# Kernel optimization log

Measured on AMD Instinct MI355X. Metric: run time of the kernel, lower is better.

## Reference

```python
import jax, jax.numpy as jnp
import numpy as np

B, L, H, NH, DH, V, NL = 256, 100, 384, 12, 32, 30000, 6
FF = 4 * H


def _gelu(x):
    c = np.sqrt(2.0 / np.pi).astype(np.float32)
    return x * (0.5 * (1.0 + jnp.tanh(c * (x + 0.044715 * x ** 3))))


def _norm(X, g, b):
    mu = jnp.mean(X, axis=2, keepdims=True)
    var = jnp.var(X, axis=2, ddof=1, keepdims=True)  # torch.var is unbiased
    return g * ((X - mu) / jnp.sqrt(var + 1e-8)) + b


def setup_inputs():
    key = jax.random.key(0)
    ks = jax.random.split(key, 24)
    s = 0.02
    return {
        'x': jax.random.randint(ks[0], (B, L), 0, V, dtype=jnp.int32),
        'seg': jax.random.randint(ks[1], (B, L), 0, 3, dtype=jnp.int32),
        'tok_emb': jax.random.uniform(ks[2], (V, H), jnp.float32, -s, s),
        'seg_emb': jax.random.uniform(ks[3], (3, H), jnp.float32, -s, s),
        'pos_emb': jax.random.normal(ks[4], (L, H), jnp.float32) * 0.05,
        'Wq': jax.random.normal(ks[5], (NL, H, H), jnp.float32) * np.sqrt(2.0 / H).astype(np.float32),
        'bq': jnp.zeros((NL, H), jnp.float32),
        'Wk': jax.random.normal(ks[6], (NL, H, H), jnp.float32) * np.sqrt(2.0 / H).astype(np.float32),
        'bk': jnp.zeros((NL, H), jnp.float32),
        'Wv': jax.random.normal(ks[7], (NL, H, H), jnp.float32) * np.sqrt(2.0 / H).astype(np.float32),
        'bv': jnp.zeros((NL, H), jnp.float32),
        'Wo': jax.random.normal(ks[8], (NL, H, H), jnp.float32) * np.sqrt(2.0 / (2 * H)).astype(np.float32),
        'bo': jnp.zeros((NL, H), jnp.float32),
        'g1': jnp.ones((NL,), jnp.float32),
        'be1': jnp.zeros((NL,), jnp.float32),
        'W1': jax.random.normal(ks[9], (NL, H, FF), jnp.float32) * np.sqrt(2.0 / (H + FF)).astype(np.float32),
        'b1': jnp.zeros((NL, FF), jnp.float32),
        'W2': jax.random.normal(ks[10], (NL, FF, H), jnp.float32) * np.sqrt(2.0 / (H + FF)).astype(np.float32),
        'b2': jnp.zeros((NL, H), jnp.float32),
        'g2': jnp.ones((NL,), jnp.float32),
        'be2': jnp.zeros((NL,), jnp.float32),
        'dropout': 0,
    }


def _encoder_layer(h, pad_mask, nonpad, Wq, bq, Wk, bk, Wv, bv, Wo, bo, g1, be1, W1, b1, W2, b2, g2, be2):
    # --- multi-head self-attention (interleaved head split, as in source) ---
    q = (h @ Wq + bq).reshape(B, L, DH, NH).transpose(3, 0, 1, 2)  # (NH,B,L,DH)
    k = (h @ Wk + bk).reshape(B, L, DH, NH).transpose(3, 0, 3 - 1, 1)  # placeholder
    k = (h @ Wk + bk).reshape(B, L, DH, NH).transpose(3, 0, 2, 1)      # (NH,B,DH,L)
    v = (h @ Wv + bv).reshape(B, L, DH, NH).transpose(3, 0, 1, 2)      # (NH,B,L,DH)
    scale = 1.0 / np.sqrt(H).astype(np.float32)  # d_k = de.shape[-1] = hidden_dim!
    e = jnp.einsum('hbld,hbdm->hblm', q, k) * scale                    # (NH,B,L,L)
    e = jnp.where(pad_mask[None], -1e10, e)
    alpha = jax.nn.softmax(e, axis=-1)
    heads = jnp.einsum('hblm,hbmd->hbld', alpha, v)                    # (NH,B,L,DH)
    a = heads.transpose(1, 2, 0, 3).reshape(B, L, H)  # cat over heads on feature dim
    attn = _norm(a @ Wo + bo + h, g1, be1)
    attn = attn * nonpad
    # --- FFN ---
    f = _gelu(attn @ W1 + b1)
    f = f @ W2 + b2
    out = _norm(f + attn, g2, be2)
    return out * nonpad


def reference(x, seg, tok_emb, seg_emb, pos_emb, Wq, bq, Wk, bk, Wv, bv, Wo, bo,
              g1, be1, W1, b1, W2, b2, g2, be2, dropout):
    pad_mask = (x == 0)[:, None, :] * jnp.ones((1, L, 1), bool)  # (B,L,L)
    nonpad = (x != 0).astype(jnp.float32)[:, :, None]            # (B,L,1), bcast over H
    h = tok_emb[x] + seg_emb[seg] + pos_emb[None, :L]
    h = h * nonpad
    acc = h  # cumulative-sum skip connections: input_i = x_i + ... + x_1
    out = h
    for i in range(NL):
        out = _encoder_layer(acc, pad_mask, nonpad,
                             Wq[i], bq[i], Wk[i], bk[i], Wv[i], bv[i], Wo[i], bo[i],
                             g1[i], be1[i], W1[i], b1[i], W2[i], b2[i], g2[i], be2[i])
        acc = acc + out
    return out
```

## Files before the change

kernel.cpp:

```cpp
#include <hip/hip_runtime.h>
#include <hip/hip_bf16.h>
#include <math.h>

#define B_  256
#define L_  100
#define H_  384
#define NH_ 12
#define DH_ 32
#define NL_ 6
#define FF_ 1536
#define M_  (B_*L_)
#define QKVN 1152

#define LW     3538944
#define OFF_Q  0
#define OFF_K  294912
#define OFF_V  589824
#define OFF_WO 884736
#define OFF_W1 1179648
#define OFF_W2 2359296

typedef __attribute__((ext_vector_type(8))) short short8;
typedef __attribute__((ext_vector_type(4))) float f32x4;

#define GLOBAL_AS __attribute__((address_space(1)))
#define LDS_AS    __attribute__((address_space(3)))

__device__ __forceinline__ void gload_lds16(const void* g, void* l) {
    __builtin_amdgcn_global_load_lds((const GLOBAL_AS void*)g, (LDS_AS void*)l, 16, 0, 0);
}

__device__ __forceinline__ void split2(float v, __hip_bfloat16& hi, __hip_bfloat16& lo) {
    hi = __float2bfloat16(v);
    lo = __float2bfloat16(v - __bfloat162float(hi));
}

__device__ __forceinline__ unsigned short f2b(float v) {
    __hip_bfloat16 h = __float2bfloat16(v);
    return *(unsigned short*)&h;
}

#define VMW(N) asm volatile("s_waitcnt vmcnt(" #N ")" ::: "memory")

__global__ void embed_kernel(const int* __restrict__ x, const int* __restrict__ seg,
                             const float* __restrict__ tok, const float* __restrict__ sege,
                             const float* __restrict__ pos,
                             __hip_bfloat16* __restrict__ acc2) {
    int idx = blockIdx.x * blockDim.x + threadIdx.x;
    if (idx >= M_ * H_) return;
    int m = idx / H_;
    int f = idx - m * H_;
    int t = x[m];
    int s = seg[m];
    int l = m % L_;
    float v = tok[t * H_ + f] + sege[s * H_ + f] + pos[l * H_ + f];
    v = (t != 0) ? v : 0.0f;
    __hip_bfloat16 h, lo;
    split2(v, h, lo);
    acc2[(size_t)m * (2 * H_) + f]      = h;
    acc2[(size_t)m * (2 * H_) + H_ + f] = lo;
}

__global__ void transpose_all_kernel(const float* __restrict__ Wq, const float* __restrict__ Wk,
        const float* __restrict__ Wv, const float* __restrict__ Wo,
        const float* __restrict__ W1, const float* __restrict__ W2,
        __hip_bfloat16* __restrict__ wT) {
    __shared__ float tile[32][33];
    int l = blockIdx.x / 1728;
    int bid = blockIdx.x % 1728;
    const float* src;
    __hip_bfloat16* dst;
    int K, N, nx, tix, perm = 0;
    if (bid < 432) {
        int m = bid / 144; tix = bid % 144;
        src = (m == 0) ? Wq : (m == 1 ? Wk : Wv);
        src += (size_t)l * H_ * H_;
        dst = wT + (size_t)l * LW + (m == 0 ? OFF_Q : (m == 1 ? OFF_K : OFF_V));
        K = 384; N = 384; nx = 12; perm = 1;
    } else if (bid < 576) {
        tix = bid - 432; src = Wo + (size_t)l * H_ * H_;
        dst = wT + (size_t)l * LW + OFF_WO; K = 384; N = 384; nx = 12;
    } else if (bid < 1152) {
        tix = bid - 576; src = W1 + (size_t)l * H_ * FF_;
        dst = wT + (size_t)l * LW + OFF_W1; K = 384; N = 1536; nx = 48;
    } else {
        tix = bid - 1152; src = W2 + (size_t)l * FF_ * H_;
        dst = wT + (size_t)l * LW + OFF_W2; K = 1536; N = 384; nx = 12;
    }
    int n0 = (tix % nx) * 32, k0 = (tix / nx) * 32;
    int tx = threadIdx.x, ty = threadIdx.y;
    #pragma unroll
    for (int i = ty; i < 32; i += 8)
        tile[i][tx] = src[(size_t)(k0 + i) * N + (n0 + tx)];
    __syncthreads();
    #pragma unroll
    for (int i = ty; i < 32; i += 8) {
        float v = tile[tx][i];
        __hip_bfloat16 h, lo;
        split2(v, h, lo);
        int j = n0 + i;
        int jo = perm ? ((j % 12) * 32 + j / 12) : j;
        dst[(size_t)jo * (2 * K) + (k0 + tx)]     = h;
        dst[(size_t)jo * (2 * K) + K + (k0 + tx)] = lo;
    }
}

__global__ void bias_concat_kernel(const float* __restrict__ bq, const float* __restrict__ bk,
                                   const float* __restrict__ bv, float* __restrict__ out) {
    int i = blockIdx.x * 256 + threadIdx.x;
    if (i >= NL_ * QKVN) return;
    int l = i / QKVN, jp = i - l * QKVN;
    int t = jp / 384, r = jp % 384;
    int h = r >> 5, d = r & 31;
    int j = d * 12 + h;
    float v = (t == 0) ? bq[l * 384 + j] : (t == 1 ? bk[l * 384 + j] : bv[l * 384 + j]);
    out[i] = v;
}

template <int TAG, int BIG, int OMODE, int MODEK, int ACT>
__global__ __launch_bounds__(BIG ? 512 : 256) void gemm_bf16_kernel(
        const __hip_bfloat16* __restrict__ A2,
        const __hip_bfloat16* __restrict__ Wt2,
        const float* __restrict__ bias,
        void* __restrict__ outp,
        int N, int K, int nbx) {
    constexpr int BM = BIG ? 256 : 128;
    __shared__ __hip_bfloat16 As[3][BM * 32];
    __shared__ __hip_bfloat16 Bs[3][128 * 32];
    int t = threadIdx.x;
    int lane = t & 63, wv = t >> 6;
    int wm = wv >> 1, wn = wv & 1;

    int nwg = gridDim.x;
    int q8 = nwg >> 3, r8 = nwg & 7;
    int xcd = blockIdx.x & 7, off = blockIdx.x >> 3;
    int swz = (xcd < r8 ? xcd * (q8 + 1) : r8 * (q8 + 1) + (xcd - r8) * q8) + off;
    int bn = (swz % nbx) * 128;
    int bm = (swz / nbx) * BM;

    const int KstA = (MODEK == 2) ? K : 2 * K;
    const int KstW = 2 * K;
    const int Kend = (MODEK == 0) ? 3 * K : 2 * K;
    f32x4 acc[4][4] = {};

    int sr   = t >> 2;
    int sswz = (t & 3) ^ ((t >> 2) & 3) ^ ((t >> 4) & 3);
    const __hip_bfloat16* a_src = A2 + (size_t)(bm + sr) * KstA + sswz * 8;
    const __hip_bfloat16* b_src = Wt2 + (size_t)(bn + sr) * KstW + sswz * 8;

    int slotp = (lane >> 4) ^ (lane & 3) ^ ((lane >> 2) & 3);
    int aOff = (wm * 64 + (lane & 15)) * 32 + slotp * 8;
    int bOff = (wn * 64 + (lane & 15)) * 32 + slotp * 8;

#define STAGE(buf, ak, wk) do { \
        gload_lds16(a_src + (ak), &As[buf][wv * 512]); \
        gload_lds16(a_src + (size_t)(BM / 2) * KstA + (ak), &As[buf][(BM / 2) * 32 + wv * 512]); \
        gload_lds16(b_src + (wk), &Bs[buf][wv * 512]); \
        if (!BIG) gload_lds16(b_src + (size_t)64 * KstW + (wk), &Bs[buf][2048 + wv * 512]); \
    } while (0)

#define KOFFS(k0, ak, wk) do { \
        if (MODEK == 0) { ak = ((k0) < K) ? (k0) : (k0) - K; wk = ((k0) < 2 * K) ? (k0) : (k0) - 2 * K; } \
        else            { ak = ((k0) < K) ? (k0) : (k0) - K; wk = (k0); } \
    } while (0)

    int nt = Kend >> 5;
    {
        int ak, wk;
        KOFFS(0, ak, wk);
        STAGE(0, ak, wk);
        KOFFS(32, ak, wk);
        STAGE(1, ak, wk);
    }
    int c0 = 0, c1 = 1, c2 = 2;
    for (int ti = 0; ti < nt; ++ti) {
        if (ti + 2 < nt) {
            int k2 = (ti + 2) << 5;
            int ak, wk;
            KOFFS(k2, ak, wk);
            STAGE(c2, ak, wk);
            if (BIG) { VMW(6); } else { VMW(8); }
        } else if (ti + 2 == nt) {
            if (BIG) { VMW(3); } else { VMW(4); }
        } else {
            VMW(0);
        }
        __builtin_amdgcn_s_barrier();
        short8 af[4], bf[4];
        #pragma unroll
        for (int m = 0; m < 4; ++m) af[m] = *(const short8*)(&As[c0][aOff + m * 512]);
        #pragma unroll
        for (int n = 0; n < 4; ++n) bf[n] = *(const short8*)(&Bs[c0][bOff + n * 512]);
        __builtin_amdgcn_s_setprio(1);
        #pragma unroll
        for (int m = 0; m < 4; ++m)
            #pragma unroll
            for (int n = 0; n < 4; ++n)
                acc[m][n] = __builtin_amdgcn_mfma_f32_16x16x32_bf16(af[m], bf[n], acc[m][n], 0, 0, 0);
        __builtin_amdgcn_s_setprio(0);
        __builtin_amdgcn_s_barrier();
        int tmp = c0; c0 = c1; c1 = c2; c2 = tmp;
    }
#undef STAGE
#undef KOFFS

    int colBase = bn + wn * 64 + (lane & 15);
    int rowBase = bm + wm * 64 + (lane >> 4) * 4;
    const float c0f = 0.7978845608f;
    #pragma unroll
    for (int n = 0; n < 4; ++n) {
        int c = colBase + n * 16;
        float bvv = bias[c];
        #pragma unroll
        for (int m = 0; m < 4; ++m) {
            int r0 = rowBase + m * 16;
            #pragma unroll
            for (int r = 0; r < 4; ++r) {
                float v = acc[m][n][r] + bvv;
                if (ACT == 1) {
                    float u = c0f * (v + 0.044715f * v * v * v);
                    v = v / (1.0f + __expf(-2.0f * u));
                }
                size_t row = (size_t)(r0 + r);
                if (OMODE == 0) {
                    ((float*)outp)[row * N + c] = v;
                } else {
                    ((__hip_bfloat16*)outp)[row * N + c] = __float2bfloat16(v);
                }
            }
        }
    }
}

__global__ __launch_bounds__(256) void attn_kernel(const __hip_bfloat16* __restrict__ qkvP,
        const int* __restrict__ x, __hip_bfloat16* __restrict__ a2) {
    __shared__ unsigned short qs[112][32];
    __shared__ unsigned short ks[128][32];
    __shared__ unsigned short vst[32][136];
    __shared__ unsigned short ps[112][136];
    __shared__ int xb[128];
    int t = threadIdx.x;
    int lane = t & 63, wv = t >> 6;
    int b = blockIdx.x / NH_;
    int nh = blockIdx.x % NH_;
    const __hip_bfloat16* base = qkvP + (size_t)b * L_ * QKVN;

    for (int i = t; i < 576; i += 256) {
        int d = i / 18, w = i % 18;
        ((int*)vst)[d * 68 + 50 + w] = 0;
    }
    for (int i = t; i < 128; i += 256) xb[i] = (i < L_) ? x[b * L_ + i] : 0;

    {
        int r16 = lane >> 2, s = lane & 3;
        for (int i = wv; i < 7; i += 4) {
            int row = i * 16 + r16;
            int sp = s ^ (row & 3) ^ ((row >> 2) & 3);
            gload_lds16(base + (size_t)row * QKVN + nh * 32 + sp * 8, &qs[i * 16][0]);
        }
        for (int i = wv; i < 8; i += 4) {
            int row = i * 16 + r16;
            int sp = s ^ (row & 3) ^ ((row >> 2) & 3);
            gload_lds16(base + (size_t)row * QKVN + 384 + nh * 32 + sp * 8, &ks[i * 16][0]);
        }
    }
    if (t < 200) {
        int kv = t >> 1, d0 = (t & 1) * 16;
        const __hip_bfloat16* vsrc = base + (size_t)kv * QKVN + 768 + nh * 32 + d0;
        short8 v0 = *(const short8*)vsrc;
        short8 v1 = *(const short8*)(vsrc + 8);
        #pragma unroll
        for (int j = 0; j < 8; ++j) {
            vst[d0 + j][kv]     = (unsigned short)v0[j];
            vst[d0 + 8 + j][kv] = (unsigned short)v1[j];
        }
    }
    __syncthreads();

    const float scale = 1.0f / sqrtf((float)H_);
    int n = lane & 15, g = lane >> 4;

    for (int rt = wv; rt < 7; rt += 4) {
        int arow = rt * 16 + n;
        int asp = (g ^ (arow & 3) ^ ((arow >> 2) & 3)) * 8;
        short8 aq = *(const short8*)&qs[arow][asp];
        f32x4 s8[8];
        #pragma unroll
        for (int ct = 0; ct < 8; ++ct) {
            int brow = ct * 16 + n;
            int bsp = (g ^ (brow & 3) ^ ((brow >> 2) & 3)) * 8;
            short8 bk = *(const short8*)&ks[brow][bsp];
            f32x4 z = {0.0f, 0.0f, 0.0f, 0.0f};
            s8[ct] = __builtin_amdgcn_mfma_f32_16x16x32_bf16(aq, bk, z, 0, 0, 0);
        }
        #pragma unroll
        for (int ct = 0; ct < 8; ++ct) {
            int col = ct * 16 + n;
            int xv = xb[col];
            #pragma unroll
            for (int r = 0; r < 4; ++r) {
                float v = s8[ct][r] * scale;
                v = (xv == 0) ? -1e10f : v;
                v = (col >= L_) ? -INFINITY : v;
                s8[ct][r] = v;
            }
        }
        float sm[4];
        #pragma unroll
        for (int r = 0; r < 4; ++r) {
            float m = s8[0][r];
            #pragma unroll
            for (int ct = 1; ct < 8; ++ct) m = fmaxf(m, s8[ct][r]);
            m = fmaxf(m, __shfl_xor(m, 1, 16));
            m = fmaxf(m, __shfl_xor(m, 2, 16));
            m = fmaxf(m, __shfl_xor(m, 4, 16));
            m = fmaxf(m, __shfl_xor(m, 8, 16));
            float s = 0.0f;
            #pragma unroll
            for (int ct = 0; ct < 8; ++ct) {
                float p = __expf(s8[ct][r] - m);
                s8[ct][r] = p;
                s += p;
            }
            s += __shfl_xor(s, 1, 16);
            s += __shfl_xor(s, 2, 16);
            s += __shfl_xor(s, 4, 16);
            s += __shfl_xor(s, 8, 16);
            sm[r] = s;
        }
        int prow = rt * 16 + g * 4;
        #pragma unroll
        for (int ct = 0; ct < 8; ++ct) {
            int col = ct * 16 + n;
            #pragma unroll
            for (int r = 0; r < 4; ++r)
                ps[prow + r][col] = f2b(s8[ct][r]);
        }
        f32x4 o0 = {0.0f, 0.0f, 0.0f, 0.0f}, o1 = o0;
        #pragma unroll
        for (int kt = 0; kt < 4; ++kt) {
            short8 pa = *(const short8*)&ps[rt * 16 + n][kt * 32 + g * 8];
            short8 b0 = *(const short8*)&vst[n][kt * 32 + g * 8];
            short8 b1 = *(const short8*)&vst[16 + n][kt * 32 + g * 8];
            o0 = __builtin_amdgcn_mfma_f32_16x16x32_bf16(pa, b0, o0, 0, 0, 0);
            o1 = __builtin_amdgcn_mfma_f32_16x16x32_bf16(pa, b1, o1, 0, 0, 0);
        }
        #pragma unroll
        for (int r = 0; r < 4; ++r) {
            int lrow = prow + r;
            if (lrow < L_) {
                size_t row = (size_t)b * L_ + lrow;
                float inv = 1.0f / sm[r];
                __hip_bfloat16 h, lo;
                float v0 = o0[r] * inv;
                split2(v0, h, lo);
                a2[row * (2 * H_) + nh * DH_ + n]      = h;
                a2[row * (2 * H_) + H_ + nh * DH_ + n] = lo;
                float v1 = o1[r] * inv;
                split2(v1, h, lo);
                a2[row * (2 * H_) + nh * DH_ + 16 + n]      = h;
                a2[row * (2 * H_) + H_ + nh * DH_ + 16 + n] = lo;
            }
        }
    }
}

template <int MODE>
__global__ __launch_bounds__(128) void ln_kernel(
        const float* __restrict__ Xf,
        const __hip_bfloat16* __restrict__ R2,
        const int* __restrict__ x,
        const float* __restrict__ gp, const float* __restrict__ bp, int layer,
        float* __restrict__ Yf,
        __hip_bfloat16* __restrict__ Y2,
        __hip_bfloat16* __restrict__ acc2) {
    int row = blockIdx.x;
    int tid = threadIdx.x;
    size_t b1 = (size_t)row * H_;
    size_t b2 = (size_t)row * (2 * H_);

    float v[3];
    #pragma unroll
    for (int j = 0; j < 3; ++j) {
        int f = tid + j * 128;
        float r = __bfloat162float(R2[b2 + f]) + __bfloat162float(R2[b2 + H_ + f]);
        v[j] = Xf[b1 + f] + r;
    }

    __shared__ float red[2];
    float s = v[0] + v[1] + v[2];
    #pragma unroll
    for (int off = 32; off > 0; off >>= 1) s += __shfl_down(s, off);
    if ((tid & 63) == 0) red[tid >> 6] = s;
    __syncthreads();
    float mu = (red[0] + red[1]) * (1.0f / 384.0f);
    __syncthreads();

    float d[3];
    float qq = 0.0f;
    #pragma unroll
    for (int j = 0; j < 3; ++j) { d[j] = v[j] - mu; qq += d[j] * d[j]; }
    #pragma unroll
    for (int off = 32; off > 0; off >>= 1) qq += __shfl_down(qq, off);
    if ((tid & 63) == 0) red[tid >> 6] = qq;
    __syncthreads();
    float var = (red[0] + red[1]) * (1.0f / 383.0f);
    float rstd = rsqrtf(var + 1e-8f);

    float g = gp[layer], bb = bp[layer];
    float np_ = (x[row] != 0) ? 1.0f : 0.0f;
    #pragma unroll
    for (int j = 0; j < 3; ++j) {
        int f = tid + j * 128;
        float y = (g * (d[j] * rstd) + bb) * np_;
        if (MODE == 0) {
            __hip_bfloat16 h, lo;
            split2(y, h, lo);
            Y2[b2 + f]      = h;
            Y2[b2 + H_ + f] = lo;
        } else {
            Yf[b1 + f] = y;
            float a = __bfloat162float(acc2[b2 + f]) + __bfloat162float(acc2[b2 + H_ + f]) + y;
            __hip_bfloat16 h, lo;
            split2(a, h, lo);
            acc2[b2 + f]      = h;
            acc2[b2 + H_ + f] = lo;
        }
    }
}

extern "C" void kernel_launch(void* const* d_in, const int* in_sizes, int n_in,
                              void* d_out, int out_size, void* d_ws, size_t ws_size,
                              hipStream_t stream) {
    const int*   x    = (const int*)d_in[0];
    const int*   seg  = (const int*)d_in[1];
    const float* tok  = (const float*)d_in[2];
    const float* sege = (const float*)d_in[3];
    const float* pos  = (const float*)d_in[4];
    const float* Wq   = (const float*)d_in[5];
    const float* bq   = (const float*)d_in[6];
    const float* Wk   = (const float*)d_in[7];
    const float* bk   = (const float*)d_in[8];
    const float* Wv   = (const float*)d_in[9];
    const float* bv   = (const float*)d_in[10];
    const float* Wo   = (const float*)d_in[11];
    const float* bo   = (const float*)d_in[12];
    const float* g1   = (const float*)d_in[13];
    const float* be1  = (const float*)d_in[14];
    const float* W1   = (const float*)d_in[15];
    const float* b1   = (const float*)d_in[16];
    const float* W2   = (const float*)d_in[17];
    const float* b2   = (const float*)d_in[18];
    const float* g2   = (const float*)d_in[19];
    const float* be2  = (const float*)d_in[20];

    char* p = (char*)d_ws;
    __hip_bfloat16* wT   = (__hip_bfloat16*)p; p += (size_t)NL_ * LW * 2;
    __hip_bfloat16* acc2 = (__hip_bfloat16*)p; p += 39321600;
    __hip_bfloat16* bE2  = (__hip_bfloat16*)p; p += 39321600;
    float* qkvb          = (float*)p;          p += 27648;
    char* pool           = p;
    __hip_bfloat16* qkvP = (__hip_bfloat16*)pool;
    __hip_bfloat16* bA2  = (__hip_bfloat16*)(pool + 58982400);
    float*          woF  = (float*)pool;
    __hip_bfloat16* f2   = (__hip_bfloat16*)pool;
    float* out = (float*)d_out;

    transpose_all_kernel<<<dim3(1728 * NL_), dim3(32, 8), 0, stream>>>(Wq, Wk, Wv, Wo, W1, W2, wT);
    bias_concat_kernel<<<dim3((NL_ * QKVN + 255) / 256), dim3(256), 0, stream>>>(bq, bk, bv, qkvb);
    embed_kernel<<<dim3((M_ * H_ + 255) / 256), dim3(256), 0, stream>>>(x, seg, tok, sege, pos, acc2);

    for (int l = 0; l < NL_; ++l) {
        const __hip_bfloat16* wTL = wT + (size_t)l * LW;
        const float* bol = bo + (size_t)l * H_;
        const float* b1l = b1 + (size_t)l * FF_;
        const float* b2l = b2 + (size_t)l * H_;

        gemm_bf16_kernel<0, 1, 2, 0, 0><<<dim3((QKVN / 128) * (M_ / 256)), dim3(512), 0, stream>>>(
            acc2, wTL + OFF_Q, qkvb + (size_t)l * QKVN, qkvP, QKVN, H_, QKVN / 128);
        attn_kernel<<<dim3(B_ * NH_), dim3(256), 0, stream>>>(qkvP, x, bA2);
        gemm_bf16_kernel<1, 0, 0, 0, 0><<<dim3((H_ / 128) * (M_ / 128)), dim3(256), 0, stream>>>(
            bA2, wTL + OFF_WO, bol, woF, H_, H_, H_ / 128);
        ln_kernel<0><<<dim3(M_), dim3(128), 0, stream>>>(
            woF, acc2, x, g1, be1, l, nullptr, bE2, nullptr);
        gemm_bf16_kernel<2, 1, 2, 0, 1><<<dim3((FF_ / 128) * (M_ / 256)), dim3(512), 0, stream>>>(
            bE2, wTL + OFF_W1, b1l, f2, FF_, H_, FF_ / 128);
        gemm_bf16_kernel<3, 1, 0, 2, 0><<<dim3((H_ / 128) * (M_ / 256)), dim3(512), 0, stream>>>(
            f2, wTL + OFF_W2, b2l, out, H_, FF_, H_ / 128);
        ln_kernel<1><<<dim3(M_), dim3(128), 0, stream>>>(
            out, bE2, x, g2, be2, l, out, nullptr, acc2);
    }
}
```

Before: 2.626 ms.

## Split-K the FFN down-projection GEMM with atomic accumulation

The W2 GEMM (K=1536, N=384) now runs as a split-K of two halves using the small 128-row tile, giving about four times as many workgroups. Each half accumulates into a fp32 output buffer through atomicAdd, and a new kernel first fills that buffer with the bias. The aim is better occupancy across the GPU for this GEMM, which has few output tiles. The cost is an extra full-size init pass, atomic traffic on the output, and a summation order that is no longer deterministic.

New measurement: 2.852 ms. 8.6% more time.

```diff
diff --git a/kernel.cpp b/kernel.cpp
--- a/kernel.cpp
+++ b/kernel.cpp
@@ -117,7 +117,12 @@
     out[i] = v;
 }
 
-template <int TAG, int BIG, int OMODE, int MODEK, int ACT>
+__global__ void initw2_kernel(const float* __restrict__ bias, float* __restrict__ out) {
+    int i = blockIdx.x * 256 + threadIdx.x;
+    if (i < M_ * H_) out[i] = bias[i % H_];
+}
+
+template <int TAG, int BIG, int OMODE, int MODEK, int ACT, int SPLITK>
 __global__ __launch_bounds__(BIG ? 512 : 256) void gemm_bf16_kernel(
         const __hip_bfloat16* __restrict__ A2,
         const __hip_bfloat16* __restrict__ Wt2,
@@ -135,6 +140,12 @@
     int q8 = nwg >> 3, r8 = nwg & 7;
     int xcd = blockIdx.x & 7, off = blockIdx.x >> 3;
     int swz = (xcd < r8 ? xcd * (q8 + 1) : r8 * (q8 + 1) + (xcd - r8) * q8) + off;
+    int half = 0;
+    if (SPLITK) {
+        int nhalf = nwg >> 1;
+        half = (swz >= nhalf) ? 1 : 0;
+        swz -= half * nhalf;
+    }
     int bn = (swz % nbx) * 128;
     int bm = (swz / nbx) * BM;
 
@@ -165,22 +176,24 @@
     } while (0)
 
     int nt = Kend >> 5;
+    int nth = SPLITK ? (nt >> 1) : nt;
+    int kb  = SPLITK ? half * (Kend >> 1) : 0;
     {
         int ak, wk;
-        KOFFS(0, ak, wk);
+        KOFFS(kb, ak, wk);
         STAGE(0, ak, wk);
-        KOFFS(32, ak, wk);
+        KOFFS(kb + 32, ak, wk);
         STAGE(1, ak, wk);
     }
     int c0 = 0, c1 = 1, c2 = 2;
-    for (int ti = 0; ti < nt; ++ti) {
-        if (ti + 2 < nt) {
-            int k2 = (ti + 2) << 5;
+    for (int ti = 0; ti < nth; ++ti) {
+        if (ti + 2 < nth) {
+            int k2 = kb + ((ti + 2) << 5);
             int ak, wk;
             KOFFS(k2, ak, wk);
             STAGE(c2, ak, wk);
             if (BIG) { VMW(6); } else { VMW(8); }
-        } else if (ti + 2 == nt) {
+        } else if (ti + 2 == nth) {
             if (BIG) { VMW(3); } else { VMW(4); }
         } else {
             VMW(0);
@@ -210,7 +223,7 @@
     #pragma unroll
     for (int n = 0; n < 4; ++n) {
         int c = colBase + n * 16;
-        float bvv = bias[c];
+        float bvv = SPLITK ? 0.0f : bias[c];
         #pragma unroll
         for (int m = 0; m < 4; ++m) {
             int r0 = rowBase + m * 16;
@@ -222,7 +235,9 @@
                     v = v / (1.0f + __expf(-2.0f * u));
                 }
                 size_t row = (size_t)(r0 + r);
-                if (OMODE == 0) {
+                if (SPLITK) {
+                    atomicAdd(&((float*)outp)[row * N + c], v);
+                } else if (OMODE == 0) {
                     ((float*)outp)[row * N + c] = v;
                 } else {
                     ((__hip_bfloat16*)outp)[row * N + c] = __float2bfloat16(v);
@@ -476,16 +491,17 @@
         const float* b1l = b1 + (size_t)l * FF_;
         const float* b2l = b2 + (size_t)l * H_;
 
-        gemm_bf16_kernel<0, 1, 2, 0, 0><<<dim3((QKVN / 128) * (M_ / 256)), dim3(512), 0, stream>>>(
+        gemm_bf16_kernel<0, 1, 2, 0, 0, 0><<<dim3((QKVN / 128) * (M_ / 256)), dim3(512), 0, stream>>>(
             acc2, wTL + OFF_Q, qkvb + (size_t)l * QKVN, qkvP, QKVN, H_, QKVN / 128);
         attn_kernel<<<dim3(B_ * NH_), dim3(256), 0, stream>>>(qkvP, x, bA2);
-        gemm_bf16_kernel<1, 0, 0, 0, 0><<<dim3((H_ / 128) * (M_ / 128)), dim3(256), 0, stream>>>(
+        gemm_bf16_kernel<1, 0, 0, 0, 0, 0><<<dim3((H_ / 128) * (M_ / 128)), dim3(256), 0, stream>>>(
             bA2, wTL + OFF_WO, bol, woF, H_, H_, H_ / 128);
         ln_kernel<0><<<dim3(M_), dim3(128), 0, stream>>>(
             woF, acc2, x, g1, be1, l, nullptr, bE2, nullptr);
-        gemm_bf16_kernel<2, 1, 2, 0, 1><<<dim3((FF_ / 128) * (M_ / 256)), dim3(512), 0, stream>>>(
+        gemm_bf16_kernel<2, 1, 2, 0, 1, 0><<<dim3((FF_ / 128) * (M_ / 256)), dim3(512), 0, stream>>>(
             bE2, wTL + OFF_W1, b1l, f2, FF_, H_, FF_ / 128);
-        gemm_bf16_kernel<3, 1, 0, 2, 0><<<dim3((H_ / 128) * (M_ / 256)), dim3(512), 0, stream>>>(
+        initw2_kernel<<<dim3((M_ * H_ + 255) / 256), dim3(256), 0, stream>>>(b2l, out);
+        gemm_bf16_kernel<3, 0, 0, 2, 0, 1><<<dim3(2 * (H_ / 128) * (M_ / 128)), dim3(256), 0, stream>>>(
             f2, wTL + OFF_W2, b2l, out, H_, FF_, H_ / 128);
         ln_kernel<1><<<dim3(M_), dim3(128), 0, stream>>>(
             out, bE2, x, g2, be2, l, out, nullptr, acc2);
```
